# Kernel tuning notes

Measured on AMD Instinct MI355X. Metric: run time of the kernel, lower is better.

The kernel has to match this reference:

```python
import jax, jax.numpy as jnp
import numpy as np

DIM = 1024
DIM_INNER = 2048
B, S = 4, 4096


def setup_inputs() -> dict:
    key = jax.random.key(0)
    k1, k2, k3 = jax.random.split(key, 3)
    x = jax.random.normal(k1, (B, S, DIM), dtype=jnp.float32)
    # torch Linear weight init ~ U(-1/sqrt(fan_in), 1/sqrt(fan_in)); scaled normals are fine
    W_hg = jax.random.normal(k2, (DIM, 2 * DIM_INNER), dtype=jnp.float32) / np.sqrt(DIM)
    W_out = jax.random.normal(k3, (DIM_INNER, DIM), dtype=jnp.float32) / np.sqrt(DIM_INNER)
    return {"x": x, "W_hg": W_hg, "W_out": W_out}


def heinsen_associative_scan_log(log_coeffs, log_values):
    # a_star[t] = sum_{i<=t} log_coeffs[i]
    a_star = jnp.cumsum(log_coeffs, axis=1)
    log_h0_plus_b_star = jax.lax.cumlogsumexp(log_values - a_star, axis=1)
    return jnp.exp(a_star + log_h0_plus_b_star)


def reference(x, W_hg, W_out):
    # fused projection then split into hidden / gate, each [B, S, DIM_INNER]
    hg = jnp.einsum('bsd,de->bse', x, W_hg)
    hidden, gate = jnp.split(hg, 2, axis=-1)
    # seq_len > 1, prev_hidden = None path of the torch module
    log_z = jax.nn.log_sigmoid(gate)                 # log sigmoid(gate)
    log_coeffs = -jax.nn.softplus(gate)              # log(1 - sigmoid(gate))
    hidden_log = jnp.log(jax.nn.relu(hidden) + 0.5)  # log(g(hidden)) as coded (relu+0.5)
    log_values = hidden_log + log_z
    h = heinsen_associative_scan_log(log_coeffs, log_values)  # [B, S, DIM_INNER]
    out = jnp.einsum('bse,ed->bsd', h, W_out)
    return out
```

## Files before the change

kernel.cpp:

```cpp
#include <hip/hip_runtime.h>
#include <stdint.h>

#define DIMX 1024
#define DIM_INNER 2048
#define BATCH 4
#define SEQ 4096
#define M_TOTAL (BATCH * SEQ)
#define N_HG (2 * DIM_INNER)
#define NCHUNK 32
#define CLEN 128

typedef unsigned short u16;
typedef __attribute__((ext_vector_type(8))) short short8;
typedef __attribute__((ext_vector_type(4))) float floatx4;

__device__ __forceinline__ float bflo(uint32_t u) { return __uint_as_float(u << 16); }
__device__ __forceinline__ float bfhi(uint32_t u) { return __uint_as_float(u & 0xffff0000u); }
__device__ __forceinline__ uint32_t f2bf_bits(float f) {
    uint32_t u = __float_as_uint(f);
    return (u + 0x7fffu + ((u >> 16) & 1u)) >> 16;
}

#define GCAST(p) (const __attribute__((address_space(1))) uint32_t*)(const void*)(p)
#define LCAST(p) (__attribute__((address_space(3))) uint32_t*)(void*)(p)
#define SYNCG(N)                                                              \
    do {                                                                      \
        asm volatile("s_waitcnt vmcnt(" #N ") lgkmcnt(0)" ::: "memory");      \
        __builtin_amdgcn_s_barrier();                                         \
    } while (0)

__global__ __launch_bounds__(256) void prep(const float* __restrict__ x,
                                            const float* __restrict__ Whg,
                                            const float* __restrict__ Wout,
                                            u16* __restrict__ xb,
                                            u16* __restrict__ whgt,
                                            u16* __restrict__ woutt) {
    __shared__ float tile[64][65];
    const int bid = blockIdx.x;
    const int tid = threadIdx.x;
    if (bid < 2048) {
        const int n4 = M_TOTAL * DIMX / 4;
        const float4* in4 = (const float4*)x;
        ushort4* out4 = (ushort4*)xb;
        for (int i = bid * 256 + tid; i < n4; i += 2048 * 256) {
            float4 v = in4[i];
            ushort4 o;
            o.x = (u16)f2bf_bits(v.x);
            o.y = (u16)f2bf_bits(v.y);
            o.z = (u16)f2bf_bits(v.z);
            o.w = (u16)f2bf_bits(v.w);
            out4[i] = o;
        }
        return;
    }
    const float* in;
    u16* out;
    int R, C, tb;
    if (bid < 3072) {
        in = Whg; out = whgt; R = DIMX; C = N_HG; tb = bid - 2048;
    } else {
        in = Wout; out = woutt; R = DIM_INNER; C = DIMX; tb = bid - 3072;
    }
    const int tilesx = C / 64;
    const int c0 = (tb % tilesx) * 64, r0 = (tb / tilesx) * 64;
    const int tx = tid & 63, ty = tid >> 6;
#pragma unroll
    for (int i = ty; i < 64; i += 4)
        tile[i][tx] = in[(size_t)(r0 + i) * C + c0 + tx];
    __syncthreads();
#pragma unroll
    for (int i = ty; i < 64; i += 4)
        out[(size_t)(c0 + i) * R + r0 + tx] = (u16)f2bf_bits(tile[tx][i]);
}

__global__ __launch_bounds__(512, 2) void gemm1_k(const u16* __restrict__ A,
                                                  const u16* __restrict__ Bt,
                                                  uint32_t* __restrict__ av,
                                                  float2* __restrict__ sumAV) {
    __shared__ alignas(16) u16 smem[65536];
    const int tid = threadIdx.x;
    const int lane = tid & 63;
    const int wave = tid >> 6;
    const int wr = wave >> 2;
    const int wc = wave & 3;
    const size_t m0 = (size_t)blockIdx.y * 256;
    const int n0 = blockIdx.x * 128;

    floatx4 acch[8][2], accg[8][2];
#pragma unroll
    for (int i = 0; i < 8; ++i)
#pragma unroll
        for (int j = 0; j < 2; ++j) {
            acch[i][j] = (floatx4){0.f, 0.f, 0.f, 0.f};
            accg[i][j] = (floatx4){0.f, 0.f, 0.f, 0.f};
        }

    const int srow = lane >> 2;
    const int ssw = ((lane & 3) ^ ((srow >> 1) & 3)) * 8;
    const u16* Ag = A + (m0 + wave * 16 + srow) * DIMX + ssw;
    const u16* Bhg = Bt + ((size_t)(n0 + wave * 16 + srow)) * DIMX + ssw;
    const u16* Bgg = Bt + ((size_t)(DIM_INNER + n0 + wave * 16 + srow)) * DIMX + ssw;

    const int fr = lane & 15;
    const int koff = ((lane >> 4) ^ ((fr >> 1) & 3)) * 8;

#define STAGE1(u)                                                                          \
    do {                                                                                   \
        const int q_ = (u) & 3;                                                            \
        const int k0_ = (u) * 32;                                                          \
        u16* b_ = smem + q_ * 16384;                                                       \
        __builtin_amdgcn_global_load_lds(GCAST(Ag + k0_), LCAST(b_ + wave * 512), 16, 0, 0);                \
        __builtin_amdgcn_global_load_lds(GCAST(Ag + (size_t)128 * DIMX + k0_),             \
                                         LCAST(b_ + 4096 + wave * 512), 16, 0, 0);         \
        __builtin_amdgcn_global_load_lds(GCAST(Bhg + k0_), LCAST(b_ + 8192 + wave * 512), 16, 0, 0);        \
        __builtin_amdgcn_global_load_lds(GCAST(Bgg + k0_), LCAST(b_ + 12288 + wave * 512), 16, 0, 0);       \
    } while (0)

#define TILE1(u, DOSTAGE)                                                                  \
    do {                                                                                   \
        const u16* As_ = smem + ((u) & 3) * 16384;                                         \
        const u16* Bh_ = As_ + 8192;                                                       \
        const u16* Bg_ = As_ + 12288;                                                      \
        short8 af_[8], bh_[2], bg_[2];                                                     \
        _Pragma("unroll") for (int j_ = 0; j_ < 2; ++j_) {                                 \
            bh_[j_] = *(const short8*)(Bh_ + (wc * 32 + j_ * 16 + fr) * 32 + koff);        \
            bg_[j_] = *(const short8*)(Bg_ + (wc * 32 + j_ * 16 + fr) * 32 + koff);        \
        }                                                                                  \
        _Pragma("unroll") for (int i_ = 0; i_ < 8; ++i_)                                   \
            af_[i_] = *(const short8*)(As_ + (wr * 128 + i_ * 16 + fr) * 32 + koff);       \
        if (DOSTAGE) STAGE1((u) + 3);                                                      \
        __builtin_amdgcn_s_setprio(1);                                                     \
        _Pragma("unroll") for (int i_ = 0; i_ < 8; ++i_)                                   \
            _Pragma("unroll") for (int j_ = 0; j_ < 2; ++j_) {                             \
                acch[i_][j_] =                                                             \
                    __builtin_amdgcn_mfma_f32_16x16x32_bf16(af_[i_], bh_[j_], acch[i_][j_], 0, 0, 0); \
                accg[i_][j_] =                                                             \
                    __builtin_amdgcn_mfma_f32_16x16x32_bf16(af_[i_], bg_[j_], accg[i_][j_], 0, 0, 0); \
            }                                                                              \
        __builtin_amdgcn_s_setprio(0);                                                     \
    } while (0)

    STAGE1(0);
    STAGE1(1);
    STAGE1(2);
    for (int t = 0; t < 29; ++t) {
        SYNCG(8);
        TILE1(t, 1);
    }
    SYNCG(8);
    TILE1(29, 0);
    SYNCG(4);
    TILE1(30, 0);
    SYNCG(0);
    TILE1(31, 0);
    __syncthreads();

    uint32_t* avl = (uint32_t*)smem;
    const int r0row = (lane >> 4) * 4;
#pragma unroll
    for (int i = 0; i < 8; ++i) {
#pragma unroll
        for (int r = 0; r < 4; ++r) {
            const int row = wr * 128 + i * 16 + r0row + r;
#pragma unroll
            for (int j = 0; j < 2; ++j) {
                const int col = wc * 32 + j * 16 + fr;
                float h = acch[i][j][r];
                float g = accg[i][j][r];
                g = fminf(fmaxf(g, -30.f), 30.f);
                float e = __expf(-g);
                float z = 1.f / (1.f + e);
                float a = e * z;
                float v = z * (fmaxf(h, 0.f) + 0.5f);
                uint32_t pk = f2bf_bits(a) | (f2bf_bits(v) << 16);
                avl[row * 128 + col] = pk;
                av[(m0 + row) * 2048 + n0 + col] = pk;
            }
        }
    }
    __syncthreads();

    const int chl = tid >> 8;
    const int t2 = tid & 255;
    const int col = t2 & 127;
    const int rlo = (t2 >> 7) * 64;
    float Aa = 1.f, Vv = 0.f;
#pragma unroll 8
    for (int j = 0; j < 64; ++j) {
        uint32_t pk = avl[(chl * 128 + rlo + j) * 128 + col];
        float a = bflo(pk), v = bfhi(pk);
        Vv = fmaf(a, Vv, v);
        Aa *= a;
    }
    __syncthreads();
    if (rlo == 0) {
        avl[chl * 256 + col] = __float_as_uint(Aa);
        avl[chl * 256 + 128 + col] = __float_as_uint(Vv);
    }
    __syncthreads();
    if (rlo != 0) {
        float Al = __uint_as_float(avl[chl * 256 + col]);
        float Vl = __uint_as_float(avl[chl * 256 + 128 + col]);
        float At = Al * Aa;
        float Vt = fmaf(Aa, Vl, Vv);
        const int chunk = (int)(m0 >> 7) + chl;
        sumAV[(size_t)chunk * 2048 + n0 + col] = (float2){At, Vt};
    }
#undef STAGE1
#undef TILE1
}

__global__ __launch_bounds__(512, 2) void gemm2_k(const u16* __restrict__ A,
                                                  const u16* __restrict__ Bt,
                                                  float* __restrict__ C) {
    const int N = DIMX, K = DIM_INNER;
    __shared__ alignas(16) u16 smem[65536];
    const int tid = threadIdx.x;
    const int lane = tid & 63;
    const int wave = tid >> 6;
    const int wr = wave >> 2;
    const int wc = wave & 3;
    const size_t m0 = (size_t)blockIdx.y * 256;
    const size_t n0 = (size_t)blockIdx.x * 256;

    floatx4 acc[8][4];
#pragma unroll
    for (int i = 0; i < 8; ++i)
#pragma unroll
        for (int j = 0; j < 4; ++j) acc[i][j] = (floatx4){0.f, 0.f, 0.f, 0.f};

    const int srow = lane >> 2;
    const int ssw = ((lane & 3) ^ ((srow >> 1) & 3)) * 8;
    const u16* Ag = A + (m0 + wave * 16 + srow) * K + ssw;
    const u16* Bg2 = Bt + (n0 + wave * 16 + srow) * K + ssw;

    const int fr = lane & 15;
    const int koff = ((lane >> 4) ^ ((fr >> 1) & 3)) * 8;

#define STAGE2(u)                                                                          \
    do {                                                                                   \
        const int q_ = (u) & 3;                                                            \
        const int k0_ = (u) * 32;                                                          \
        u16* b_ = smem + q_ * 16384;                                                       \
        __builtin_amdgcn_global_load_lds(GCAST(Ag + k0_), LCAST(b_ + wave * 512), 16, 0, 0);            \
        __builtin_amdgcn_global_load_lds(GCAST(Ag + (size_t)128 * K + k0_),                \
                                         LCAST(b_ + 4096 + wave * 512), 16, 0, 0);         \
        __builtin_amdgcn_global_load_lds(GCAST(Bg2 + k0_), LCAST(b_ + 8192 + wave * 512), 16, 0, 0);    \
        __builtin_amdgcn_global_load_lds(GCAST(Bg2 + (size_t)128 * K + k0_),               \
                                         LCAST(b_ + 12288 + wave * 512), 16, 0, 0);        \
    } while (0)

#define TILE2(u, DOSTAGE)                                                                  \
    do {                                                                                   \
        const u16* As_ = smem + ((u) & 3) * 16384;                                         \
        const u16* Bs_ = As_ + 8192;                                                       \
        short8 af_[8], bf_[4];                                                             \
        _Pragma("unroll") for (int j_ = 0; j_ < 4; ++j_)                                   \
            bf_[j_] = *(const short8*)(Bs_ + (wc * 64 + j_ * 16 + fr) * 32 + koff);        \
        _Pragma("unroll") for (int i_ = 0; i_ < 8; ++i_)                                   \
            af_[i_] = *(const short8*)(As_ + (wr * 128 + i_ * 16 + fr) * 32 + koff);       \
        if (DOSTAGE) STAGE2((u) + 3);                                                      \
        __builtin_amdgcn_s_setprio(1);                                                     \
        _Pragma("unroll") for (int i_ = 0; i_ < 8; ++i_)                                   \
            _Pragma("unroll") for (int j_ = 0; j_ < 4; ++j_)                               \
                acc[i_][j_] =                                                              \
                    __builtin_amdgcn_mfma_f32_16x16x32_bf16(af_[i_], bf_[j_], acc[i_][j_], 0, 0, 0); \
        __builtin_amdgcn_s_setprio(0);                                                     \
    } while (0)

    STAGE2(0);
    STAGE2(1);
    STAGE2(2);
    for (int t = 0; t < 61; ++t) {
        SYNCG(8);
        TILE2(t, 1);
    }
    SYNCG(8);
    TILE2(61, 0);
    SYNCG(4);
    TILE2(62, 0);
    SYNCG(0);
    TILE2(63, 0);

    const int r0row = (lane >> 4) * 4;
#pragma unroll
    for (int i = 0; i < 8; ++i)
#pragma unroll
        for (int r = 0; r < 4; ++r) {
            size_t row = m0 + wr * 128 + i * 16 + r0row + r;
#pragma unroll
            for (int j = 0; j < 4; ++j) {
                size_t col = n0 + wc * 64 + j * 16 + fr;
                C[row * N + col] = acc[i][j][r];
            }
        }
#undef STAGE2
#undef TILE2
}

__global__ __launch_bounds__(64) void scan_carry(const float2* __restrict__ sumAV,
                                                 float* __restrict__ carry) {
    const int g = blockIdx.x * 64 + threadIdx.x;
    const int b = g >> 11, c = g & 2047;
    float h = 0.f;
#pragma unroll 8
    for (int ch = 0; ch < NCHUNK; ++ch) {
        float2 s = sumAV[(size_t)(b * NCHUNK + ch) * 2048 + c];
        carry[(size_t)(b * NCHUNK + ch) * 2048 + c] = h;
        h = fmaf(s.x, h, s.y);
    }
}

__global__ __launch_bounds__(256) void scan_apply(const uint32_t* __restrict__ av,
                                                  const float* __restrict__ carry,
                                                  uint32_t* __restrict__ hbuf) {
    const int b = blockIdx.z, ch = blockIdx.y;
    const int c2 = blockIdx.x * 256 + threadIdx.x;
    const size_t rowbase = (size_t)b * SEQ + (size_t)ch * CLEN;
    const uint32_t* p = av + rowbase * 2048 + c2 * 2;
    uint32_t* q = hbuf + rowbase * 1024 + c2;
    const float2 cin = ((const float2*)carry)[(size_t)(b * NCHUNK + ch) * 1024 + c2];
    float h0 = cin.x, h1 = cin.y;

    uint2 buf[4];
#pragma unroll
    for (int t = 0; t < 4; ++t) buf[t] = *(const uint2*)(p + (size_t)t * 2048);

    for (int j0 = 0; j0 < CLEN; j0 += 4) {
        uint2 nxt[4];
        if (j0 + 4 < CLEN) {
#pragma unroll
            for (int t = 0; t < 4; ++t)
                nxt[t] = *(const uint2*)(p + (size_t)(j0 + 4 + t) * 2048);
        }
#pragma unroll
        for (int t = 0; t < 4; ++t) {
            float a0 = bflo(buf[t].x), v0 = bfhi(buf[t].x);
            float a1 = bflo(buf[t].y), v1 = bfhi(buf[t].y);
            h0 = fmaf(a0, h0, v0);
            h1 = fmaf(a1, h1, v1);
            q[(size_t)(j0 + t) * 1024] = f2bf_bits(h0) | (f2bf_bits(h1) << 16);
        }
#pragma unroll
        for (int t = 0; t < 4; ++t) buf[t] = nxt[t];
    }
}

extern "C" void kernel_launch(void* const* d_in, const int* in_sizes, int n_in,
                              void* d_out, int out_size, void* d_ws, size_t ws_size,
                              hipStream_t stream) {
    const float* x = (const float*)d_in[0];
    const float* Whg = (const float*)d_in[1];
    const float* Wout = (const float*)d_in[2];

    char* ws = (char*)d_ws;
    size_t off = 0;
    u16* xb = (u16*)(ws + off);        off += (size_t)M_TOTAL * DIMX * 2;
    u16* whgt = (u16*)(ws + off);      off += (size_t)N_HG * DIMX * 2;
    u16* woutt = (u16*)(ws + off);     off += (size_t)DIMX * DIM_INNER * 2;
    uint32_t* av = (uint32_t*)(ws + off); off += (size_t)M_TOTAL * DIM_INNER * 4;
    uint32_t* hbuf = (uint32_t*)(ws + off); off += (size_t)M_TOTAL * DIM_INNER * 2;
    float2* sumAV = (float2*)(ws + off); off += (size_t)BATCH * NCHUNK * DIM_INNER * 8;
    float* carry = (float*)whgt;

    prep<<<2048 + 1024 + 512, 256, 0, stream>>>(x, Whg, Wout, xb, whgt, woutt);

    gemm1_k<<<dim3(16, 64), 512, 0, stream>>>(xb, whgt, av, sumAV);

    scan_carry<<<128, 64, 0, stream>>>(sumAV, carry);
    scan_apply<<<dim3(4, NCHUNK, BATCH), 256, 0, stream>>>(av, carry, hbuf);

    gemm2_k<<<dim3(DIMX / 256, M_TOTAL / 256), 512, 0, stream>>>((const u16*)hbuf, woutt, (float*)d_out);
}
```

Baseline: 393.4 us.

## Restructure GEMM mainloops into double-buffered K=64 tiles with interleaved sub-stage loads

```diff
diff --git a/kernel.cpp b/kernel.cpp
--- a/kernel.cpp
+++ b/kernel.cpp
@@ -23,11 +23,18 @@
 
 #define GCAST(p) (const __attribute__((address_space(1))) uint32_t*)(const void*)(p)
 #define LCAST(p) (__attribute__((address_space(3))) uint32_t*)(void*)(p)
-#define SYNCG(N)                                                              \
-    do {                                                                      \
-        asm volatile("s_waitcnt vmcnt(" #N ") lgkmcnt(0)" ::: "memory");      \
-        __builtin_amdgcn_s_barrier();                                         \
-    } while (0)
+#define BAR()                                          \
+    do {                                               \
+        __builtin_amdgcn_s_barrier();                  \
+        asm volatile("" ::: "memory");                 \
+    } while (0)
+#define LGKM0()                                                  \
+    do {                                                         \
+        asm volatile("s_waitcnt lgkmcnt(0)" ::: "memory");       \
+        __builtin_amdgcn_sched_barrier(0);                       \
+    } while (0)
+#define VMCNT_(n) asm volatile("s_waitcnt vmcnt(" #n ")" ::: "memory")
+#define VMCNT(n) VMCNT_(n)
 
 __global__ __launch_bounds__(256) void prep(const float* __restrict__ x,
                                             const float* __restrict__ Whg,
@@ -77,14 +84,16 @@
                                                   const u16* __restrict__ Bt,
                                                   uint32_t* __restrict__ av,
                                                   float2* __restrict__ sumAV) {
-    __shared__ alignas(16) u16 smem[65536];
+    __shared__ alignas(16) u16 smem16[65536];
     const int tid = threadIdx.x;
     const int lane = tid & 63;
-    const int wave = tid >> 6;
-    const int wr = wave >> 2;
-    const int wc = wave & 3;
+    const int w = tid >> 6;
+    const int wr = w >> 2;
+    const int wc = w & 3;
     const size_t m0 = (size_t)blockIdx.y * 256;
     const int n0 = blockIdx.x * 128;
+#define X1 0
+#define Y1 32768
 
     floatx4 acch[8][2], accg[8][2];
 #pragma unroll
@@ -95,67 +104,118 @@
             accg[i][j] = (floatx4){0.f, 0.f, 0.f, 0.f};
         }
 
-    const int srow = lane >> 2;
-    const int ssw = ((lane & 3) ^ ((srow >> 1) & 3)) * 8;
-    const u16* Ag = A + (m0 + wave * 16 + srow) * DIMX + ssw;
-    const u16* Bhg = Bt + ((size_t)(n0 + wave * 16 + srow)) * DIMX + ssw;
-    const u16* Bgg = Bt + ((size_t)(DIM_INNER + n0 + wave * 16 + srow)) * DIMX + ssw;
-
     const int fr = lane & 15;
-    const int koff = ((lane >> 4) ^ ((fr >> 1) & 3)) * 8;
-
-#define STAGE1(u)                                                                          \
-    do {                                                                                   \
-        const int q_ = (u) & 3;                                                            \
-        const int k0_ = (u) * 32;                                                          \
-        u16* b_ = smem + q_ * 16384;                                                       \
-        __builtin_amdgcn_global_load_lds(GCAST(Ag + k0_), LCAST(b_ + wave * 512), 16, 0, 0);                \
-        __builtin_amdgcn_global_load_lds(GCAST(Ag + (size_t)128 * DIMX + k0_),             \
-                                         LCAST(b_ + 4096 + wave * 512), 16, 0, 0);         \
-        __builtin_amdgcn_global_load_lds(GCAST(Bhg + k0_), LCAST(b_ + 8192 + wave * 512), 16, 0, 0);        \
-        __builtin_amdgcn_global_load_lds(GCAST(Bgg + k0_), LCAST(b_ + 12288 + wave * 512), 16, 0, 0);       \
-    } while (0)
-
-#define TILE1(u, DOSTAGE)                                                                  \
-    do {                                                                                   \
-        const u16* As_ = smem + ((u) & 3) * 16384;                                         \
-        const u16* Bh_ = As_ + 8192;                                                       \
-        const u16* Bg_ = As_ + 12288;                                                      \
-        short8 af_[8], bh_[2], bg_[2];                                                     \
-        _Pragma("unroll") for (int j_ = 0; j_ < 2; ++j_) {                                 \
-            bh_[j_] = *(const short8*)(Bh_ + (wc * 32 + j_ * 16 + fr) * 32 + koff);        \
-            bg_[j_] = *(const short8*)(Bg_ + (wc * 32 + j_ * 16 + fr) * 32 + koff);        \
-        }                                                                                  \
-        _Pragma("unroll") for (int i_ = 0; i_ < 8; ++i_)                                   \
-            af_[i_] = *(const short8*)(As_ + (wr * 128 + i_ * 16 + fr) * 32 + koff);       \
-        if (DOSTAGE) STAGE1((u) + 3);                                                      \
-        __builtin_amdgcn_s_setprio(1);                                                     \
-        _Pragma("unroll") for (int i_ = 0; i_ < 8; ++i_)                                   \
-            _Pragma("unroll") for (int j_ = 0; j_ < 2; ++j_) {                             \
-                acch[i_][j_] =                                                             \
-                    __builtin_amdgcn_mfma_f32_16x16x32_bf16(af_[i_], bh_[j_], acch[i_][j_], 0, 0, 0); \
-                accg[i_][j_] =                                                             \
-                    __builtin_amdgcn_mfma_f32_16x16x32_bf16(af_[i_], bg_[j_], accg[i_][j_], 0, 0, 0); \
-            }                                                                              \
-        __builtin_amdgcn_s_setprio(0);                                                     \
-    } while (0)
-
-    STAGE1(0);
-    STAGE1(1);
-    STAGE1(2);
-    for (int t = 0; t < 29; ++t) {
-        SYNCG(8);
-        TILE1(t, 1);
-    }
-    SYNCG(8);
-    TILE1(29, 0);
-    SYNCG(4);
-    TILE1(30, 0);
-    SYNCG(0);
-    TILE1(31, 0);
+    const int kb = lane >> 4;
+    const int sw0 = kb ^ (fr & 7);
+    const int a0 = (wr * 128 + fr) * 64 + sw0 * 8;
+    const int a1 = a0 ^ 32;
+    const int b0 = 16384 + (wc * 32 + fr) * 64 + sw0 * 8;
+    const int b1 = b0 ^ 32;
+
+    const int sr = lane >> 3;
+    const int sswz = (lane & 7) ^ sr;
+    const u16* pA = A + (m0 + w * 8 + sr) * DIMX + sswz * 8;
+    const u16* pBh = Bt + ((size_t)(n0 + w * 8 + sr)) * DIMX + sswz * 8;
+    const u16* pBg = pBh + (size_t)DIM_INNER * DIMX;
+
+#define ST1A(bufb, kt, h, l)                                                        \
+    __builtin_amdgcn_global_load_lds(                                               \
+        GCAST(pA + (size_t)((h) * 128 + (l) * 64) * DIMX + (kt) * 64),              \
+        LCAST(smem16 + (bufb) + (h) * 8192 + (l) * 4096 + w * 512), 16, 0, 0)
+#define ST1H(bufb, kt, l)                                                           \
+    __builtin_amdgcn_global_load_lds(                                               \
+        GCAST(pBh + (size_t)((l) * 64) * DIMX + (kt) * 64),                         \
+        LCAST(smem16 + (bufb) + 16384 + (l) * 4096 + w * 512), 16, 0, 0)
+#define ST1G(bufb, kt, l)                                                           \
+    __builtin_amdgcn_global_load_lds(                                               \
+        GCAST(pBg + (size_t)((l) * 64) * DIMX + (kt) * 64),                         \
+        LCAST(smem16 + (bufb) + 24576 + (l) * 4096 + w * 512), 16, 0, 0)
+
+#define LDS8(idx) (*(const short8*)(smem16 + (idx)))
+    short8 af[2][4], bh[2][2], bg[2][2];
+#define RDA1(bufb, mh)                                                  \
+    do {                                                                \
+        _Pragma("unroll") for (int i_ = 0; i_ < 4; ++i_) {              \
+            af[0][i_] = LDS8((bufb) + a0 + ((mh) * 4 + i_) * 1024);     \
+            af[1][i_] = LDS8((bufb) + a1 + ((mh) * 4 + i_) * 1024);     \
+        }                                                               \
+    } while (0)
+#define RDBH1(bufb)                                                     \
+    do {                                                                \
+        _Pragma("unroll") for (int j_ = 0; j_ < 2; ++j_) {              \
+            bh[0][j_] = LDS8((bufb) + b0 + j_ * 1024);                  \
+            bh[1][j_] = LDS8((bufb) + b1 + j_ * 1024);                  \
+        }                                                               \
+    } while (0)
+#define RDBG1(bufb)                                                     \
+    do {                                                                \
+        _Pragma("unroll") for (int j_ = 0; j_ < 2; ++j_) {              \
+            bg[0][j_] = LDS8((bufb) + b0 + 8192 + j_ * 1024);           \
+            bg[1][j_] = LDS8((bufb) + b1 + 8192 + j_ * 1024);           \
+        }                                                               \
+    } while (0)
+#define MM1(ACC, IB, BF)                                                                     \
+    do {                                                                                     \
+        __builtin_amdgcn_s_setprio(1);                                                       \
+        _Pragma("unroll") for (int i_ = 0; i_ < 4; ++i_)                                     \
+            _Pragma("unroll") for (int j_ = 0; j_ < 2; ++j_) {                               \
+            ACC[(IB) + i_][j_] = __builtin_amdgcn_mfma_f32_16x16x32_bf16(                    \
+                af[0][i_], BF[0][j_], ACC[(IB) + i_][j_], 0, 0, 0);                          \
+            ACC[(IB) + i_][j_] = __builtin_amdgcn_mfma_f32_16x16x32_bf16(                    \
+                af[1][i_], BF[1][j_], ACC[(IB) + i_][j_], 0, 0, 0);                          \
+        }                                                                                    \
+        __builtin_amdgcn_s_setprio(0);                                                       \
+    } while (0)
+
+#define ITER1(t, FULL, G4, G8)                                                               \
+    do {                                                                                     \
+                                                            \
+        RDA1(X1, 0); RDBH1(X1);                                                              \
+        ST1A(Y1, (t) + 1, 1, 0); ST1A(Y1, (t) + 1, 1, 1);                                    \
+        BAR(); LGKM0(); MM1(acch, 0, bh); BAR();                                             \
+                                                                          \
+        RDBG1(X1);                                                                           \
+        if (FULL) { ST1H(X1, (t) + 2, 0); ST1H(X1, (t) + 2, 1); }                            \
+        BAR(); LGKM0(); MM1(accg, 0, bg); BAR();                                             \
+                                                                          \
+        RDA1(X1, 1);                                                                         \
+        if (FULL) { ST1G(X1, (t) + 2, 0); ST1G(X1, (t) + 2, 1); }                            \
+        BAR(); LGKM0(); MM1(acch, 4, bh); BAR();                                             \
+                                                                    \
+        if (FULL) { ST1A(X1, (t) + 2, 0, 0); ST1A(X1, (t) + 2, 0, 1); }                      \
+        VMCNT(G4); BAR(); MM1(accg, 4, bg); BAR();                                           \
+                                                          \
+        RDA1(Y1, 0); RDBH1(Y1);                                                              \
+        if (FULL) { ST1A(X1, (t) + 2, 1, 0); ST1A(X1, (t) + 2, 1, 1); }                      \
+        BAR(); LGKM0(); MM1(acch, 0, bh); BAR();                                             \
+                                                                          \
+        RDBG1(Y1);                                                                           \
+        if (FULL) { ST1H(Y1, (t) + 3, 0); ST1H(Y1, (t) + 3, 1); }                            \
+        BAR(); LGKM0(); MM1(accg, 0, bg); BAR();                                             \
+                                                                          \
+        RDA1(Y1, 1);                                                                         \
+        if (FULL) { ST1G(Y1, (t) + 3, 0); ST1G(Y1, (t) + 3, 1); }                            \
+        BAR(); LGKM0(); MM1(acch, 4, bh); BAR();                                             \
+                                                                    \
+        if (FULL) { ST1A(Y1, (t) + 3, 0, 0); ST1A(Y1, (t) + 3, 0, 1); }                      \
+        VMCNT(G8); BAR(); MM1(accg, 4, bg); BAR();                                           \
+    } while (0)
+
+    ST1H(X1, 0, 0); ST1H(X1, 0, 1);
+    ST1G(X1, 0, 0); ST1G(X1, 0, 1);
+    ST1A(X1, 0, 0, 0); ST1A(X1, 0, 0, 1);
+    ST1A(X1, 0, 1, 0); ST1A(X1, 0, 1, 1);
+    ST1H(Y1, 1, 0); ST1H(Y1, 1, 1);
+    ST1G(Y1, 1, 0); ST1G(Y1, 1, 1);
+    ST1A(Y1, 1, 0, 0); ST1A(Y1, 1, 0, 1);
+    VMCNT(6); BAR();
+#pragma unroll 1
+    for (int it = 0; it < 7; ++it) ITER1(2 * it, 1, 6, 6);
+    ITER1(14, 0, 0, 6);
+
     __syncthreads();
 
-    uint32_t* avl = (uint32_t*)smem;
+    uint32_t* avl = (uint32_t*)smem16;
     const int r0row = (lane >> 4) * 4;
 #pragma unroll
     for (int i = 0; i < 8; ++i) {
@@ -206,20 +266,26 @@
         const int chunk = (int)(m0 >> 7) + chl;
         sumAV[(size_t)chunk * 2048 + n0 + col] = (float2){At, Vt};
     }
-#undef STAGE1
-#undef TILE1
+#undef ST1A
+#undef ST1H
+#undef ST1G
+#undef RDA1
+#undef RDBH1
+#undef RDBG1
+#undef MM1
+#undef ITER1
 }
 
 __global__ __launch_bounds__(512, 2) void gemm2_k(const u16* __restrict__ A,
                                                   const u16* __restrict__ Bt,
                                                   float* __restrict__ C) {
     const int N = DIMX, K = DIM_INNER;
-    __shared__ alignas(16) u16 smem[65536];
+    __shared__ alignas(16) u16 smem16[65536];
     const int tid = threadIdx.x;
     const int lane = tid & 63;
-    const int wave = tid >> 6;
-    const int wr = wave >> 2;
-    const int wc = wave & 3;
+    const int w = tid >> 6;
+    const int wr = w >> 2;
+    const int wc = w & 3;
     const size_t m0 = (size_t)blockIdx.y * 256;
     const size_t n0 = (size_t)blockIdx.x * 256;
 
@@ -229,58 +295,94 @@
 #pragma unroll
         for (int j = 0; j < 4; ++j) acc[i][j] = (floatx4){0.f, 0.f, 0.f, 0.f};
 
-    const int srow = lane >> 2;
-    const int ssw = ((lane & 3) ^ ((srow >> 1) & 3)) * 8;
-    const u16* Ag = A + (m0 + wave * 16 + srow) * K + ssw;
-    const u16* Bg2 = Bt + (n0 + wave * 16 + srow) * K + ssw;
-
     const int fr = lane & 15;
-    const int koff = ((lane >> 4) ^ ((fr >> 1) & 3)) * 8;
-
-#define STAGE2(u)                                                                          \
-    do {                                                                                   \
-        const int q_ = (u) & 3;                                                            \
-        const int k0_ = (u) * 32;                                                          \
-        u16* b_ = smem + q_ * 16384;                                                       \
-        __builtin_amdgcn_global_load_lds(GCAST(Ag + k0_), LCAST(b_ + wave * 512), 16, 0, 0);            \
-        __builtin_amdgcn_global_load_lds(GCAST(Ag + (size_t)128 * K + k0_),                \
-                                         LCAST(b_ + 4096 + wave * 512), 16, 0, 0);         \
-        __builtin_amdgcn_global_load_lds(GCAST(Bg2 + k0_), LCAST(b_ + 8192 + wave * 512), 16, 0, 0);    \
-        __builtin_amdgcn_global_load_lds(GCAST(Bg2 + (size_t)128 * K + k0_),               \
-                                         LCAST(b_ + 12288 + wave * 512), 16, 0, 0);        \
-    } while (0)
-
-#define TILE2(u, DOSTAGE)                                                                  \
-    do {                                                                                   \
-        const u16* As_ = smem + ((u) & 3) * 16384;                                         \
-        const u16* Bs_ = As_ + 8192;                                                       \
-        short8 af_[8], bf_[4];                                                             \
-        _Pragma("unroll") for (int j_ = 0; j_ < 4; ++j_)                                   \
-            bf_[j_] = *(const short8*)(Bs_ + (wc * 64 + j_ * 16 + fr) * 32 + koff);        \
-        _Pragma("unroll") for (int i_ = 0; i_ < 8; ++i_)                                   \
-            af_[i_] = *(const short8*)(As_ + (wr * 128 + i_ * 16 + fr) * 32 + koff);       \
-        if (DOSTAGE) STAGE2((u) + 3);                                                      \
-        __builtin_amdgcn_s_setprio(1);                                                     \
-        _Pragma("unroll") for (int i_ = 0; i_ < 8; ++i_)                                   \
-            _Pragma("unroll") for (int j_ = 0; j_ < 4; ++j_)                               \
-                acc[i_][j_] =                                                              \
-                    __builtin_amdgcn_mfma_f32_16x16x32_bf16(af_[i_], bf_[j_], acc[i_][j_], 0, 0, 0); \
-        __builtin_amdgcn_s_setprio(0);                                                     \
-    } while (0)
-
-    STAGE2(0);
-    STAGE2(1);
-    STAGE2(2);
-    for (int t = 0; t < 61; ++t) {
-        SYNCG(8);
-        TILE2(t, 1);
-    }
-    SYNCG(8);
-    TILE2(61, 0);
-    SYNCG(4);
-    TILE2(62, 0);
-    SYNCG(0);
-    TILE2(63, 0);
+    const int kb = lane >> 4;
+    const int sw0 = kb ^ (fr & 7);
+    const int a0 = (wr * 128 + fr) * 64 + sw0 * 8;
+    const int a1 = a0 ^ 32;
+    const int b0 = 16384 + (wc * 64 + fr) * 64 + sw0 * 8;
+    const int b1 = b0 ^ 32;
+
+    const int sr = lane >> 3;
+    const int sswz = (lane & 7) ^ sr;
+    const u16* pA = A + (m0 + w * 8 + sr) * K + sswz * 8;
+    const u16* pB = Bt + (n0 + w * 8 + sr) * K + sswz * 8;
+
+#define ST2A(bufb, kt, h, l)                                                        \
+    __builtin_amdgcn_global_load_lds(                                               \
+        GCAST(pA + (size_t)((h) * 128 + (l) * 64) * K + (kt) * 64),                 \
+        LCAST(smem16 + (bufb) + (h) * 8192 + (l) * 4096 + w * 512), 16, 0, 0)
+#define ST2B(bufb, kt, h, l)                                                        \
+    __builtin_amdgcn_global_load_lds(                                               \
+        GCAST(pB + (size_t)((h) * 128 + (l) * 64) * K + (kt) * 64),                 \
+        LCAST(smem16 + (bufb) + 16384 + (h) * 8192 + (l) * 4096 + w * 512), 16, 0, 0)
+
+    short8 af[2][4], ba[2][2], bb[2][2];
+#define RDA2(bufb, mh)                                                  \
+    do {                                                                \
+        _Pragma("unroll") for (int i_ = 0; i_ < 4; ++i_) {              \
+            af[0][i_] = LDS8((bufb) + a0 + ((mh) * 4 + i_) * 1024);     \
+            af[1][i_] = LDS8((bufb) + a1 + ((mh) * 4 + i_) * 1024);     \
+        }                                                               \
+    } while (0)
+#define RDB2(bufb, BF, nh)                                                  \
+    do {                                                                    \
+        _Pragma("unroll") for (int j_ = 0; j_ < 2; ++j_) {                  \
+            BF[0][j_] = LDS8((bufb) + b0 + ((nh) * 2 + j_) * 1024);         \
+            BF[1][j_] = LDS8((bufb) + b1 + ((nh) * 2 + j_) * 1024);         \
+        }                                                                   \
+    } while (0)
+#define MM2(IB, JB, BF)                                                                      \
+    do {                                                                                     \
+        __builtin_amdgcn_s_setprio(1);                                                       \
+        _Pragma("unroll") for (int i_ = 0; i_ < 4; ++i_)                                     \
+            _Pragma("unroll") for (int j_ = 0; j_ < 2; ++j_) {                               \
+            acc[(IB) + i_][(JB) + j_] = __builtin_amdgcn_mfma_f32_16x16x32_bf16(             \
+                af[0][i_], BF[0][j_], acc[(IB) + i_][(JB) + j_], 0, 0, 0);                   \
+            acc[(IB) + i_][(JB) + j_] = __builtin_amdgcn_mfma_f32_16x16x32_bf16(             \
+                af[1][i_], BF[1][j_], acc[(IB) + i_][(JB) + j_], 0, 0, 0);                   \
+        }                                                                                    \
+        __builtin_amdgcn_s_setprio(0);                                                       \
+    } while (0)
+
+#define ITER2(t, FULL, G4, G8)                                                               \
+    do {                                                                                     \
+         RDA2(X1, 0); RDB2(X1, ba, 0);                                              \
+        ST2A(Y1, (t) + 1, 0, 0); ST2A(Y1, (t) + 1, 0, 1);                                    \
+        BAR(); LGKM0(); MM2(0, 0, ba); BAR();                                                \
+         RDB2(X1, bb, 1);                                                           \
+        ST2A(Y1, (t) + 1, 1, 0); ST2A(Y1, (t) + 1, 1, 1);                                    \
+        BAR(); LGKM0(); MM2(0, 2, bb); BAR();                                                \
+         RDA2(X1, 1);                                                               \
+        if (FULL) { ST2B(X1, (t) + 2, 0, 0); ST2B(X1, (t) + 2, 0, 1); }                      \
+        BAR(); LGKM0(); MM2(4, 0, ba); BAR();                                                \
+                                                                                    \
+        if (FULL) { ST2B(X1, (t) + 2, 1, 0); ST2B(X1, (t) + 2, 1, 1); }                      \
+        VMCNT(G4); BAR(); MM2(4, 2, bb); BAR();                                              \
+         RDA2(Y1, 0); RDB2(Y1, ba, 0);                                              \
+        if (FULL) { ST2A(X1, (t) + 2, 0, 0); ST2A(X1, (t) + 2, 0, 1); }                      \
+        BAR(); LGKM0(); MM2(0, 0, ba); BAR();                                                \
+         RDB2(Y1, bb, 1);                                                           \
+        if (FULL) { ST2A(X1, (t) + 2, 1, 0); ST2A(X1, (t) + 2, 1, 1); }                      \
+        BAR(); LGKM0(); MM2(0, 2, bb); BAR();                                                \
+         RDA2(Y1, 1);                                                               \
+        if (FULL) { ST2B(Y1, (t) + 3, 0, 0); ST2B(Y1, (t) + 3, 0, 1); }                      \
+        BAR(); LGKM0(); MM2(4, 0, ba); BAR();                                                \
+                                                                                    \
+        if (FULL) { ST2B(Y1, (t) + 3, 1, 0); ST2B(Y1, (t) + 3, 1, 1); }                      \
+        VMCNT(G8); BAR(); MM2(4, 2, bb); BAR();                                              \
+    } while (0)
+
+    ST2B(X1, 0, 0, 0); ST2B(X1, 0, 0, 1);
+    ST2B(X1, 0, 1, 0); ST2B(X1, 0, 1, 1);
+    ST2A(X1, 0, 0, 0); ST2A(X1, 0, 0, 1);
+    ST2A(X1, 0, 1, 0); ST2A(X1, 0, 1, 1);
+    ST2B(Y1, 1, 0, 0); ST2B(Y1, 1, 0, 1);
+    ST2B(Y1, 1, 1, 0); ST2B(Y1, 1, 1, 1);
+    VMCNT(4); BAR();
+#pragma unroll 1
+    for (int it = 0; it < 15; ++it) ITER2(2 * it, 1, 4, 4);
+    ITER2(30, 0, 0, 4);
 
     const int r0row = (lane >> 4) * 4;
 #pragma unroll
@@ -294,8 +396,12 @@
                 C[row * N + col] = acc[i][j][r];
             }
         }
-#undef STAGE2
-#undef TILE2
+#undef ST2A
+#undef ST2B
+#undef RDA2
+#undef RDB2
+#undef MM2
+#undef ITER2
 }
 
 __global__ __launch_bounds__(64) void scan_carry(const float2* __restrict__ sumAV,
```

Result: faster. 376.0 us (-4.4%).
